# Kernel tuning notes

Measured on AMD Instinct MI355X. Metric: run time of the kernel, lower is better.

## Reference

```python
import jax, jax.numpy as jnp
import numpy as np

B = 16384
N_NODES = 55
N = B * N_NODES
IN_CH = 13
HID = 32
MAX_NBR = 6
N_LAYERS = 5
E = 4 * N


def _sage(x, src, dst, wl, bl, wr, n):
    # PyG SAGEConv: out = lin_l(mean_j x_j) + lin_r(x_i); lin_l has bias, lin_r does not.
    msgs = x[src]                                                   # [E, d]
    agg = jax.ops.segment_sum(msgs, dst, num_segments=n)            # [N, d]
    cnt = jax.ops.segment_sum(jnp.ones((src.shape[0],), x.dtype), dst, num_segments=n)
    agg = agg / jnp.maximum(cnt, 1.0)[:, None]
    return agg @ wl + bl + x @ wr


def setup_inputs() -> dict:
    key = jax.random.key(0)
    ks = jax.random.split(key, 24)
    x = jax.random.normal(ks[0], (N, IN_CH), dtype=jnp.float32)
    # column -3 (index 10) is a binary neighbor mask: exactly MAX_NBR ones per graph
    u = jax.random.uniform(ks[1], (B, N_NODES))
    nbr_idx = jnp.argsort(u, axis=1)[:, :MAX_NBR]
    mask = jnp.zeros((B, N_NODES), jnp.float32).at[jnp.arange(B)[:, None], nbr_idx].set(1.0)
    x = x.at[:, IN_CH - 3].set(mask.reshape(-1))
    edge_index = jax.random.randint(ks[2], (2, E), 0, N, dtype=jnp.int64)
    shuffle_indices = jax.random.randint(ks[3], (B, MAX_NBR), 0, MAX_NBR, dtype=jnp.int64)
    s = 0.1
    wl0 = jax.random.normal(ks[4], (IN_CH, HID)) * s
    bl0 = jnp.zeros((HID,), jnp.float32)
    wr0 = jax.random.normal(ks[5], (IN_CH, HID)) * s
    wl = jax.random.normal(ks[6], (N_LAYERS - 1, HID, HID)) * s
    bl = jnp.zeros((N_LAYERS - 1, HID), jnp.float32)
    wr = jax.random.normal(ks[7], (N_LAYERS - 1, HID, HID)) * s
    wq = jax.random.normal(ks[8], (HID, HID)) * s
    bq = jnp.zeros((HID,), jnp.float32)
    wk = jax.random.normal(ks[9], (HID, HID)) * s
    bk = jnp.zeros((HID,), jnp.float32)
    wv = jax.random.normal(ks[10], (HID, HID)) * s
    bv = jnp.zeros((HID,), jnp.float32)
    wo = jax.random.normal(ks[11], (HID, HID)) * s
    bo = jnp.zeros((HID,), jnp.float32)
    w_fc = jax.random.normal(ks[12], (HID * MAX_NBR, MAX_NBR)) * s
    b_fc = jnp.zeros((MAX_NBR,), jnp.float32)
    return {"x": x, "edge_index": edge_index, "shuffle_indices": shuffle_indices,
            "wl0": wl0, "bl0": bl0, "wr0": wr0, "wl": wl, "bl": bl, "wr": wr,
            "wq": wq, "bq": bq, "wk": wk, "bk": bk, "wv": wv, "bv": bv,
            "wo": wo, "bo": bo, "w_fc": w_fc, "b_fc": b_fc}


def reference(x, edge_index, shuffle_indices, wl0, bl0, wr0, wl, bl, wr,
              wq, bq, wk, bk, wv, bv, wo, bo, w_fc, b_fc):
    n = x.shape[0]
    b = n // N_NODES
    src, dst = edge_index[0], edge_index[1]
    nbr_mask = x[:, IN_CH - 3].reshape(b, N_NODES)                  # [B, 55]

    h = jax.nn.selu(_sage(x, src, dst, wl0, bl0, wr0, n))
    jk = h
    for i in range(N_LAYERS - 1):
        h = jax.nn.selu(_sage(h, src, dst, wl[i], bl[i], wr[i], n))
        jk = jnp.maximum(jk, h)                                     # JumpingKnowledge('max')

    h = jax.nn.selu(jk)                                             # [N, HID]
    keys = h.reshape(b, N_NODES, HID)
    values = keys

    # dynamic neighbor gather: indices of mask==1 in ascending order, zero-padded to MAX_NBR
    order = jnp.argsort(-nbr_mask, axis=1, stable=True)[:, :MAX_NBR]  # [B, 6]
    barange = jnp.arange(b)[:, None]
    query = keys[barange, order]                                    # [B, 6, HID]
    valid = jnp.take_along_axis(nbr_mask, order, axis=1) > 0.5      # [B, 6] bool
    query = jnp.where(valid[..., None], query, 0.0)
    query = query[barange, shuffle_indices]                         # shuffled gather

    # single-head cross attention (head_dim = HID)
    Q = query @ wq + bq
    K = keys @ wk + bk
    V = values @ wv + bv
    scores = jnp.einsum('bqd,bkd->bqk', Q, K) / jnp.sqrt(jnp.float32(HID))
    attn = jax.nn.softmax(scores, axis=-1)
    out = jnp.einsum('bqk,bkd->bqd', attn, V) @ wo + bo             # [B, 6, HID]

    out = jax.nn.selu(out.reshape(b, HID * MAX_NBR))
    return out @ w_fc + b_fc                                        # [B, 6]
```

## Files before the change

kernel.cpp:

```cpp
#include <hip/hip_runtime.h>
#include <cstdint>
#include <cstddef>

#define NODES   55
#define BGRAPH  16384
#define NTOT    (BGRAPH*NODES)
#define INCH    13
#define HID     32
#define ETOT    (4*NTOT)
#define NPB     128
#define ECAP    768
#define ZN      NTOT

#define NBUCK   220
#define BSH     12
#define BMSK    4095
#define NBLK    2048
#define BCAP2   32
#define BINTH   256
#define BINGRP  (ETOT/4/NBLK)
#define OVFCAP  8192

#define ASTR    72
#define BSTR    72
#define ASTR0   40
#define WKV_OFF 9216

#define MODE_A  0
#define MODE_D  2
#define MODE_B  3
#define MODE_C  4

typedef _Float16 f16;
typedef _Float16 f16x4 __attribute__((ext_vector_type(4)));
typedef _Float16 f16x8 __attribute__((ext_vector_type(8)));
typedef float    f32x4 __attribute__((ext_vector_type(4)));
typedef uint32_t u32x4 __attribute__((ext_vector_type(4)));

__device__ __forceinline__ float selu_f(float v){
  const float s  = 1.0507009873554805f;
  const float sa = 1.7580993408473766f;
  return v > 0.f ? s*v : sa*(__expf(v)-1.f);
}

__global__ __launch_bounds__(256) void k_pad(const float* __restrict__ x,
                                             f16* __restrict__ xh,
                                             f16* __restrict__ ha,
                                             f16* __restrict__ hb,
                                             int* __restrict__ ocnt){
  if (blockIdx.x == 0){
    int t = threadIdx.x;
    if (t == 0) *ocnt = 0;
    if (t < 16)                  xh[(size_t)ZN*16 + t]      = (f16)0.f;
    else if (t >= 16 && t < 48)  ha[(size_t)ZN*32 + (t-16)] = (f16)0.f;
    else if (t >= 48 && t < 80)  hb[(size_t)ZN*32 + (t-48)] = (f16)0.f;
  }
  int i = blockIdx.x*256 + threadIdx.x;
  int node = i>>2, q = i&3;
  const float* r = x + (size_t)node*INCH + q*4;
  f16x4 v;
  v[0] = (f16)r[0];
  v[1] = (q<3) ? (f16)r[1] : (f16)0.f;
  v[2] = (q<3) ? (f16)r[2] : (f16)0.f;
  v[3] = (q<3) ? (f16)r[3] : (f16)0.f;
  *(f16x4*)(xh + (size_t)node*16 + q*4) = v;
}

__global__ __launch_bounds__(256) void k_wprep(
    const float* __restrict__ wl0, const float* __restrict__ wr0,
    const float* __restrict__ wl,  const float* __restrict__ wr,
    const float* __restrict__ wk,  const float* __restrict__ wv,
    f16* __restrict__ wcp)
{
  int t = threadIdx.x;
  for (int i=t; i<1024; i+=256){
    int oc = i>>5, k = i&31;
    float v = 0.f;
    if (k < 13)                 v = wl0[k*HID + oc];
    else if (k >= 16 && k < 29) v = wr0[(k-16)*HID + oc];
    wcp[oc*32 + k] = (f16)v;
  }
  for (int i=t; i<4*2048; i+=256){
    int l = i>>11, r = i&2047, oc = r>>6, k = r&63;
    float v = (k<32) ? wl[l*1024 + k*HID + oc] : wr[l*1024 + (k-32)*HID + oc];
    wcp[1024 + l*2048 + oc*64 + k] = (f16)v;
  }
  for (int i=t; i<2048; i+=256){
    int oc = i>>5, k = i&31;
    float v = (oc < 32) ? wk[k*HID + oc] : wv[k*HID + (oc-32)];
    wcp[WKV_OFF + oc*32 + k] = (f16)v;
  }
}

__global__ __launch_bounds__(BINTH) void k_bin(
    const int* __restrict__ src, const int* __restrict__ dst,
    uint32_t* __restrict__ binned, int* __restrict__ gcnt,
    uint2* __restrict__ ovf, int* __restrict__ ocnt)
{
  __shared__ int lcnt[NBUCK];
  int t = threadIdx.x, bid = blockIdx.x;
  for (int i=t;i<NBUCK;i+=BINTH) lcnt[i]=0;
  __syncthreads();
  const int4* s4 = (const int4*)src;
  const int4* d4 = (const int4*)dst;
  int g0 = bid*BINGRP;
  for (int i=t; i<BINGRP; i+=BINTH){
    int4 s = s4[g0+i];
    int4 d = d4[g0+i];
    #pragma unroll
    for (int j=0;j<4;j++){
      int dd = (&d.x)[j];
      int ss = (&s.x)[j];
      int b  = dd >> BSH;
      uint32_t entry = (uint32_t)ss | ((uint32_t)(dd & BMSK) << 20);
      int pos = atomicAdd(&lcnt[b], 1);
      if (pos < BCAP2) binned[((size_t)b*NBLK + bid)*BCAP2 + pos] = entry;
      else {
        int gp = atomicAdd(ocnt, 1);
        if (gp < OVFCAP) ovf[gp] = make_uint2(entry, (uint32_t)b);
      }
    }
  }
  __syncthreads();
  for (int i=t;i<NBUCK;i+=BINTH){
    int c = lcnt[i]; if (c > BCAP2) c = BCAP2;
    gcnt[bid*NBUCK + i] = c;
  }
}

__global__ __launch_bounds__(256) void k_btot(const int* __restrict__ gcnt,
                                              const uint2* __restrict__ ovf,
                                              const int* __restrict__ ocnt,
                                              int* __restrict__ btot){
  __shared__ int sd[256];
  int b = blockIdx.x, t = threadIdx.x;
  int s = 0;
  for (int i=t;i<NBLK;i+=256) s += gcnt[i*NBUCK + b];
  int oc = *ocnt; if (oc > OVFCAP) oc = OVFCAP;
  for (int j=t;j<oc;j+=256) if (ovf[j].y == (uint32_t)b) s++;
  sd[t]=s; __syncthreads();
  for (int o=128;o>0;o>>=1){ if (t<o) sd[t]+=sd[t+o]; __syncthreads(); }
  if (t==0) btot[b]=sd[0];
}

__global__ __launch_bounds__(256) void k_bscan(const int* __restrict__ btot,
                                               int* __restrict__ bbase){
  __shared__ int sd[256];
  int t = threadIdx.x;
  int v = (t<NBUCK) ? btot[t] : 0;
  sd[t] = v; __syncthreads();
  for (int o=1;o<256;o<<=1){
    int u = (t>=o) ? sd[t-o] : 0;
    __syncthreads();
    sd[t] += u;
    __syncthreads();
  }
  if (t<NBUCK) bbase[t] = sd[t] - v;
}

__global__ __launch_bounds__(1024) void k_bucket(
    const uint32_t* __restrict__ binned, const int* __restrict__ gcnt,
    const int* __restrict__ bbase,
    const uint2* __restrict__ ovf, const int* __restrict__ ocnt,
    int* __restrict__ off, uint32_t* __restrict__ csrp)
{
  __shared__ int hist[4096];
  __shared__ int cnts[NBLK];
  __shared__ int ws[1024];
  int b = blockIdx.x, t = threadIdx.x;
  int base = bbase[b];
  for (int i=t;i<NBLK;i+=1024) cnts[i] = gcnt[i*NBUCK + b];
  #pragma unroll
  for (int i=0;i<4;i++) hist[t+1024*i] = 0;
  int oc = *ocnt; if (oc > OVFCAP) oc = OVFCAP;
  __syncthreads();

  const uint4* bb4 = (const uint4*)(binned + (size_t)b*(NBLK*BCAP2));
  for (int i=t; i<NBLK*BCAP2/4; i+=1024){
    uint4 e = bb4[i];
    int c = cnts[i>>3];
    int s0 = (i&7)*4;
    if (s0   < c) atomicAdd(&hist[(e.x>>20)&BMSK],1);
    if (s0+1 < c) atomicAdd(&hist[(e.y>>20)&BMSK],1);
    if (s0+2 < c) atomicAdd(&hist[(e.z>>20)&BMSK],1);
    if (s0+3 < c) atomicAdd(&hist[(e.w>>20)&BMSK],1);
  }
  for (int j=t;j<oc;j+=1024){
    uint2 pr = ovf[j];
    if (pr.y == (uint32_t)b) atomicAdd(&hist[(pr.x>>20)&BMSK],1);
  }
  __syncthreads();
  int t4 = t*4;
  int s0=hist[t4], s1=hist[t4+1], s2=hist[t4+2], s3=hist[t4+3];
  int sum = s0+s1+s2+s3;
  ws[t] = sum; __syncthreads();
  for (int o=1;o<1024;o<<=1){
    int u = (t>=o) ? ws[t-o] : 0;
    __syncthreads();
    ws[t] += u;
    __syncthreads();
  }
  int ex = ws[t] - sum;
  int p0 = ex, p1 = ex+s0, p2 = ex+s0+s1, p3 = ex+s0+s1+s2;
  hist[t4]=p0; hist[t4+1]=p1; hist[t4+2]=p2; hist[t4+3]=p3;
  int4 ov; ov.x = base+p0; ov.y = base+p1; ov.z = base+p2; ov.w = base+p3;
  ((int4*)(off + (b<<BSH)))[t] = ov;
  if (b == NBUCK-1 && t == 1023) off[NTOT] = ETOT;
  __syncthreads();
  for (int i=t; i<NBLK*BCAP2/4; i+=1024){
    uint4 e = bb4[i];
    int c = cnts[i>>3];
    int s0b = (i&7)*4;
    int p;
    if (s0b   < c){ p = atomicAdd(&hist[(e.x>>20)&BMSK],1); csrp[base+p] = e.x & 0xFFFFFu; }
    if (s0b+1 < c){ p = atomicAdd(&hist[(e.y>>20)&BMSK],1); csrp[base+p] = e.y & 0xFFFFFu; }
    if (s0b+2 < c){ p = atomicAdd(&hist[(e.z>>20)&BMSK],1); csrp[base+p] = e.z & 0xFFFFFu; }
    if (s0b+3 < c){ p = atomicAdd(&hist[(e.w>>20)&BMSK],1); csrp[base+p] = e.w & 0xFFFFFu; }
  }
  for (int j=t;j<oc;j+=1024){
    uint2 pr = ovf[j];
    if (pr.y == (uint32_t)b){
      int p = atomicAdd(&hist[(pr.x>>20)&BMSK],1);
      csrp[base+p] = pr.x & 0xFFFFFu;
    }
  }
}

__global__ __launch_bounds__(256,8) void k_layer0(
    const f16* __restrict__ xh,
    const int* __restrict__ off, const uint32_t* __restrict__ csrp,
    const f16* __restrict__ wcat0, const float* __restrict__ bl0,
    f16* __restrict__ hout)
{
  __shared__ uint32_t ALDS[NPB*(ASTR0/2)];
  __shared__ uint32_t BLDS[32*(ASTR0/2)];
  __shared__ uint32_t EL[ECAP];
  __shared__ int      sOFF[NPB+2];
  __shared__ float    biasL[32];
  int t = threadIdx.x;
  int base = blockIdx.x*NPB;
  int e0 = off[base];
  int e1 = off[base+NPB];
  for (int i=t; i<NPB+1; i+=256) sOFF[i] = off[base+i];
  {
    int lim = (e1-e0) < ECAP ? (e1-e0) : ECAP;
    for (int i=t; i<lim; i+=256) EL[i] = csrp[e0+i];
  }
  if (t < 128){
    int oc = t>>2, kq = (t&3)*8;
    f16x8 wv = *(const f16x8*)(wcat0 + oc*32 + kq);
    *(f16x8*)((f16*)BLDS + oc*ASTR0 + kq) = wv;
  }
  if (t < 32) biasL[t] = bl0[t];
  __syncthreads();

  int c4 = t & 3;
  #pragma unroll
  for (int p=0;p<2;p++){
    int nl = p*64 + (t>>2);
    int node = base + nl;
    f16x4 xown = *(const f16x4*)(xh + (size_t)node*16 + 4u*c4);
    int s = sOFF[nl] - e0;
    int d = sOFF[nl+1] - sOFF[nl];
    float a0=0.f,a1=0.f,a2=0.f,a3=0.f;
    for (int i=0;i<d;i+=4){
      int j0 = s+i;
      uint32_t k0,k1,k2,k3;
      if (j0+3 < ECAP){ k0=EL[j0]; k1=EL[j0+1]; k2=EL[j0+2]; k3=EL[j0+3]; }
      else            { k0=csrp[e0+j0]; k1=csrp[e0+j0+1]; k2=csrp[e0+j0+2]; k3=csrp[e0+j0+3]; }
      k1 = (i+1<d)?k1:(uint32_t)ZN;
      k2 = (i+2<d)?k2:(uint32_t)ZN;
      k3 = (i+3<d)?k3:(uint32_t)ZN;
      f16x4 g0 = *(const f16x4*)(xh + (size_t)k0*16u + 4u*c4);
      f16x4 g1 = *(const f16x4*)(xh + (size_t)k1*16u + 4u*c4);
      f16x4 g2 = *(const f16x4*)(xh + (size_t)k2*16u + 4u*c4);
      f16x4 g3 = *(const f16x4*)(xh + (size_t)k3*16u + 4u*c4);
      a0 += ((float)g0[0]+(float)g1[0]) + ((float)g2[0]+(float)g3[0]);
      a1 += ((float)g0[1]+(float)g1[1]) + ((float)g2[1]+(float)g3[1]);
      a2 += ((float)g0[2]+(float)g1[2]) + ((float)g2[2]+(float)g3[2]);
      a3 += ((float)g0[3]+(float)g1[3]) + ((float)g2[3]+(float)g3[3]);
    }
    float inv = 1.f/(float)(d<1?1:d);
    union { f16 h[4]; uint32_t u[2]; } mp, xp;
    mp.h[0]=(f16)(a0*inv); mp.h[1]=(f16)(a1*inv); mp.h[2]=(f16)(a2*inv); mp.h[3]=(f16)(a3*inv);
    xp.h[0]=xown[0]; xp.h[1]=xown[1]; xp.h[2]=xown[2]; xp.h[3]=xown[3];
    uint32_t* arow = &ALDS[nl*(ASTR0/2)];
    *((uint2*)&arow[2*c4])     = make_uint2(mp.u[0], mp.u[1]);
    *((uint2*)&arow[8 + 2*c4]) = make_uint2(xp.u[0], xp.u[1]);
  }
  __syncthreads();

  int w = t>>6, l = t&63;
  int lrow = l&15, lg = l>>4;
  const f16* Af = (const f16*)ALDS;
  const f16* Bf = (const f16*)BLDS;
  f32x4 D00={0.f,0.f,0.f,0.f}, D01=D00, D10=D00, D11=D00;
  {
    f16x8 af0 = *(const f16x8*)(Af + (32*w+lrow)*ASTR0    + 8*lg);
    f16x8 af1 = *(const f16x8*)(Af + (32*w+16+lrow)*ASTR0 + 8*lg);
    f16x8 bf0 = *(const f16x8*)(Bf + lrow*ASTR0           + 8*lg);
    f16x8 bf1 = *(const f16x8*)(Bf + (16+lrow)*ASTR0      + 8*lg);
    D00 = __builtin_amdgcn_mfma_f32_16x16x32_f16(af0, bf0, D00, 0,0,0);
    D01 = __builtin_amdgcn_mfma_f32_16x16x32_f16(af0, bf1, D01, 0,0,0);
    D10 = __builtin_amdgcn_mfma_f32_16x16x32_f16(af1, bf0, D10, 0,0,0);
    D11 = __builtin_amdgcn_mfma_f32_16x16x32_f16(af1, bf1, D11, 0,0,0);
  }
  __syncthreads();

  f16* ST = (f16*)ALDS;
  #pragma unroll
  for (int j=0;j<4;j++){
    int r0 = 32*w + 4*lg + j, r1 = r0 + 16;
    ST[r0*34 + lrow]      = (f16)selu_f(D00[j] + biasL[lrow]);
    ST[r0*34 + 16 + lrow] = (f16)selu_f(D01[j] + biasL[16+lrow]);
    ST[r1*34 + lrow]      = (f16)selu_f(D10[j] + biasL[lrow]);
    ST[r1*34 + 16 + lrow] = (f16)selu_f(D11[j] + biasL[16+lrow]);
  }
  __syncthreads();

  const uint32_t* STd = (const uint32_t*)ALDS;
  uint4* ho4 = (uint4*)hout;
  int gbase = blockIdx.x*(NPB*HID/8);
  #pragma unroll
  for (int k=0;k<2;k++){
    int cch = t + 256*k;
    int n = cch>>2, m = cch&3;
    int dd = n*17 + m*4;
    uint4 u;
    u.x=STd[dd]; u.y=STd[dd+1]; u.z=STd[dd+2]; u.w=STd[dd+3];
    ho4[gbase+cch] = u;
  }
}

__global__ __launch_bounds__(256,6) void k_layer(
    const f16* __restrict__ hin,
    const int* __restrict__ off, const uint32_t* __restrict__ csrp,
    const f16* __restrict__ wcat, const float* __restrict__ bl,
    f16* __restrict__ hout, f16* __restrict__ jkio, int mode)
{
  __shared__ uint32_t ALDS[NPB*(ASTR/2)];
  __shared__ uint32_t BLDS[32*(BSTR/2)];
  __shared__ uint32_t EL[ECAP];
  __shared__ int      sOFF[NPB+2];
  __shared__ float    biasL[32];
  int t = threadIdx.x;
  int base = blockIdx.x*NPB;
  int e0 = off[base];
  int e1 = off[base+NPB];
  for (int i=t; i<NPB+1; i+=256) sOFF[i] = off[base+i];
  {
    int lim = (e1-e0) < ECAP ? (e1-e0) : ECAP;
    for (int i=t; i<lim; i+=256) EL[i] = csrp[e0+i];
  }
  if (t < 128){
    int oc = t>>2, kq = (t&3)*8;
    f16x8 wv0 = *(const f16x8*)(wcat + oc*64 + kq);
    f16x8 wv1 = *(const f16x8*)(wcat + oc*64 + 32 + kq);
    *(f16x8*)((f16*)BLDS + oc*BSTR + kq)      = wv0;
    *(f16x8*)((f16*)BLDS + oc*BSTR + 32 + kq) = wv1;
  }
  if (t < 32) biasL[t] = bl[t];
  __syncthreads();

  int c4 = t & 3;
  #pragma unroll
  for (int p=0;p<2;p++){
    int nl = p*64 + (t>>2);
    int node = base + nl;
    f16x8 hown = *(const f16x8*)(hin + (size_t)node*HID + 8u*c4);
    int s = sOFF[nl] - e0;
    int d = sOFF[nl+1] - sOFF[nl];
    float a[8];
    #pragma unroll
    for (int r=0;r<8;r++) a[r]=0.f;
    for (int i=0;i<d;i+=4){
      int j0 = s+i;
      uint32_t k0,k1,k2,k3;
      if (j0+3 < ECAP){ k0=EL[j0]; k1=EL[j0+1]; k2=EL[j0+2]; k3=EL[j0+3]; }
      else            { k0=csrp[e0+j0]; k1=csrp[e0+j0+1]; k2=csrp[e0+j0+2]; k3=csrp[e0+j0+3]; }
      k1 = (i+1<d)?k1:(uint32_t)ZN;
      k2 = (i+2<d)?k2:(uint32_t)ZN;
      k3 = (i+3<d)?k3:(uint32_t)ZN;
      f16x8 g0 = *((const f16x8*)(hin + (size_t)k0*32u) + c4);
      f16x8 g1 = *((const f16x8*)(hin + (size_t)k1*32u) + c4);
      f16x8 g2 = *((const f16x8*)(hin + (size_t)k2*32u) + c4);
      f16x8 g3 = *((const f16x8*)(hin + (size_t)k3*32u) + c4);
      #pragma unroll
      for (int r=0;r<8;r++)
        a[r] += ((float)g0[r]+(float)g1[r]) + ((float)g2[r]+(float)g3[r]);
    }
    float inv = 1.f/(float)(d<1?1:d);
    union { f16 h[8]; uint4 v; } mp;
    #pragma unroll
    for (int r=0;r<8;r++) mp.h[r] = (f16)(a[r]*inv);
    uint32_t* arow = &ALDS[nl*(ASTR/2)];
    *((uint4*)&arow[4*c4]) = mp.v;
    *((f16x8*)((f16*)arow + 32 + 8*c4)) = hown;
  }
  __syncthreads();

  int w = t>>6, l = t&63;
  int lrow = l&15, lg = l>>4;
  const f16* Af = (const f16*)ALDS;
  const f16* Bf = (const f16*)BLDS;
  f32x4 D00={0.f,0.f,0.f,0.f}, D01=D00, D10=D00, D11=D00;
  #pragma unroll
  for (int s2=0;s2<2;s2++){
    f16x8 af0 = *(const f16x8*)(Af + (32*w+lrow)*ASTR    + 32*s2 + 8*lg);
    f16x8 af1 = *(const f16x8*)(Af + (32*w+16+lrow)*ASTR + 32*s2 + 8*lg);
    f16x8 bf0 = *(const f16x8*)(Bf + lrow*BSTR           + 32*s2 + 8*lg);
    f16x8 bf1 = *(const f16x8*)(Bf + (16+lrow)*BSTR      + 32*s2 + 8*lg);
    D00 = __builtin_amdgcn_mfma_f32_16x16x32_f16(af0, bf0, D00, 0,0,0);
    D01 = __builtin_amdgcn_mfma_f32_16x16x32_f16(af0, bf1, D01, 0,0,0);
    D10 = __builtin_amdgcn_mfma_f32_16x16x32_f16(af1, bf0, D10, 0,0,0);
    D11 = __builtin_amdgcn_mfma_f32_16x16x32_f16(af1, bf1, D11, 0,0,0);
  }
  __syncthreads();

  f16* ST = (f16*)ALDS;
  #pragma unroll
  for (int j=0;j<4;j++){
    int r0 = 32*w + 4*lg + j, r1 = r0 + 16;
    ST[r0*34 + lrow]      = (f16)selu_f(D00[j] + biasL[lrow]);
    ST[r0*34 + 16 + lrow] = (f16)selu_f(D01[j] + biasL[16+lrow]);
    ST[r1*34 + lrow]      = (f16)selu_f(D10[j] + biasL[lrow]);
    ST[r1*34 + 16 + lrow] = (f16)selu_f(D11[j] + biasL[16+lrow]);
  }
  __syncthreads();

  const uint32_t* STd = (const uint32_t*)ALDS;
  u32x4* ho4 = (u32x4*)hout;
  u32x4* jo4 = (u32x4*)jkio;
  const u32x4* hi4 = (const u32x4*)hin;
  int gbase = blockIdx.x*(NPB*HID/8);
  #pragma unroll
  for (int k=0;k<2;k++){
    int cch = t + 256*k;
    int n = cch>>2, m = cch&3;
    int dd = n*17 + m*4;
    union UU { u32x4 u; f16 hh[8]; };
    UU hv, jv, j2;
    hv.u = (u32x4){STd[dd], STd[dd+1], STd[dd+2], STd[dd+3]};
    if (mode != MODE_B){
      if (mode == MODE_A) jv.u = hi4[gbase+cch];
      else                jv.u = __builtin_nontemporal_load(jo4 + gbase + cch);
      if (mode == MODE_C){
        j2.u = hi4[gbase+cch];
        #pragma unroll
        for (int r=0;r<8;r++) jv.hh[r] = (j2.hh[r] > jv.hh[r]) ? j2.hh[r] : jv.hh[r];
      }
      #pragma unroll
      for (int r=0;r<8;r++) jv.hh[r] = (hv.hh[r] > jv.hh[r]) ? hv.hh[r] : jv.hh[r];
      __builtin_nontemporal_store(jv.u, jo4 + gbase + cch);
    }
    if (mode != MODE_D) ho4[gbase+cch] = hv.u;
  }
}

__global__ __launch_bounds__(256) void k_attn(
    const f16* __restrict__ jk, const float* __restrict__ x,
    const int* __restrict__ shuf, const f16* __restrict__ wkvT,
    const float* __restrict__ wq, const float* __restrict__ bq,
    const float* __restrict__ bk, const float* __restrict__ bv,
    const float* __restrict__ wo, const float* __restrict__ bo,
    const float* __restrict__ wfc, const float* __restrict__ bfc,
    float* __restrict__ out)
{
  __shared__ alignas(16) f16 Ah[64*40];
  __shared__ float K[NODES*33];
  __shared__ float V[NODES*33];
  __shared__ float Qs[6*33];
  __shared__ float S[6*56];
  __shared__ float O[6*33];
  __shared__ float SO[192];
  __shared__ float part[96];
  __shared__ int   sel[8];

  int g = blockIdx.x, t = threadIdx.x;

  {
    const f16x8* j8 = (const f16x8*)(jk + (size_t)g*NODES*HID);
    for (int i=t; i<NODES*HID/8; i+=256){
      f16x8 v = __builtin_nontemporal_load(j8 + i);
      int node = i >> 2, c0 = (i & 3)*8;
      f16x8 hv;
      #pragma unroll
      for (int r=0;r<8;r++) hv[r] = (f16)selu_f((float)v[r]);
      *(f16x8*)(Ah + node*40 + c0) = hv;
    }
  }
  if (t < 64){
    float mv = (t < NODES) ? x[(size_t)(g*NODES+t)*INCH + (INCH-3)] : 0.f;
    unsigned long long mb = __ballot(mv > 0.5f);
    if (t < 6){
      int kk = shuf[g*6 + t];
      for (int i2=0;i2<kk;i2++) mb &= (mb - 1ull);
      sel[t] = (int)__builtin_ctzll(mb);
    }
  }
  __syncthreads();

  {
    int w = t>>6, l = t&63;
    int lrow = l&15, lg = l>>4;
    f16x8 af = *(const f16x8*)(Ah + (16*w + lrow)*40 + 8*lg);
    #pragma unroll
    for (int ct=0; ct<4; ct++){
      f16x8 bf = *(const f16x8*)(wkvT + (16*ct + lrow)*32 + 8*lg);
      f32x4 D = {0.f,0.f,0.f,0.f};
      D = __builtin_amdgcn_mfma_f32_16x16x32_f16(af, bf, D, 0,0,0);
      int ocl = 16*(ct&1) + lrow;
      float bias = (ct < 2) ? bk[ocl] : bv[ocl];
      float* dst = (ct < 2) ? K : V;
      #pragma unroll
      for (int j=0;j<4;j++){
        int node = 16*w + 4*lg + j;
        if (node < NODES) dst[node*33 + ocl] = D[j] + bias;
      }
    }
  }
  if (t < 192){
    int q = t>>5, oc = t&31;
    int node = sel[q];
    const f16x8* hr8 = (const f16x8*)(Ah + node*40);
    float a = bq[oc];
    #pragma unroll
    for (int cc=0;cc<4;cc++){
      f16x8 hv = hr8[cc];
      #pragma unroll
      for (int r=0;r<8;r++) a = fmaf((float)hv[r], wq[(8*cc+r)*HID + oc], a);
    }
    Qs[q*33+oc] = a;
  }
  __syncthreads();

  for (int idx=t; idx<6*NODES; idx+=256){
    int q = idx % 6, k = idx / 6;
    float a = 0.f;
    #pragma unroll
    for (int c=0;c<HID;c++) a = fmaf(Qs[q*33+c], K[k*33+c], a);
    S[q*56+k] = a * 0.17677669529663687f;
  }
  __syncthreads();

  if (t < 192){
    int q = t>>5, l = t&31;
    float v0 = (l      < NODES) ? S[q*56+l]    : -1e30f;
    float v1 = (l+32   < NODES) ? S[q*56+l+32] : -1e30f;
    float mx = fmaxf(v0, v1);
    #pragma unroll
    for (int o=16;o>0;o>>=1) mx = fmaxf(mx, __shfl_xor(mx, o, 32));
    float p0 = (l    < NODES) ? __expf(v0-mx) : 0.f;
    float p1 = (l+32 < NODES) ? __expf(v1-mx) : 0.f;
    float sm = p0 + p1;
    #pragma unroll
    for (int o=16;o>0;o>>=1) sm += __shfl_xor(sm, o, 32);
    float inv = 1.f/sm;
    if (l    < NODES) S[q*56+l]    = p0*inv;
    if (l+32 < NODES) S[q*56+l+32] = p1*inv;
  }
  __syncthreads();

  if (t < 192){
    int q = t>>5, oc = t&31;
    float a = 0.f;
    for (int k=0;k<NODES;k++) a = fmaf(S[q*56+k], V[k*33+oc], a);
    O[q*33+oc] = a;
  }
  __syncthreads();

  if (t < 192){
    int q = t>>5, oc = t&31;
    float a = bo[oc];
    #pragma unroll
    for (int c=0;c<HID;c++) a = fmaf(O[q*33+c], wo[c*HID+oc], a);
    SO[t] = selu_f(a);
  }
  __syncthreads();

  if (t < 96){
    int j = t % 6, pp = t / 6;
    float a = 0.f;
    #pragma unroll
    for (int r=0;r<12;r++) a = fmaf(SO[pp*12+r], wfc[(pp*12+r)*6+j], a);
    part[pp*6+j] = a;
  }
  __syncthreads();
  if (t < 6){
    float a = bfc[t];
    #pragma unroll
    for (int pp=0;pp<16;pp++) a += part[pp*6+t];
    out[g*6+t] = a;
  }
}

extern "C" void kernel_launch(void* const* d_in, const int* in_sizes, int n_in,
                              void* d_out, int out_size, void* d_ws, size_t ws_size,
                              hipStream_t stream)
{
  const float* x   = (const float*)d_in[0];
  const int*   eix = (const int*)d_in[1];
  const int*   shf = (const int*)d_in[2];
  const float* wl0 = (const float*)d_in[3];
  const float* bl0 = (const float*)d_in[4];
  const float* wr0 = (const float*)d_in[5];
  const float* wl  = (const float*)d_in[6];
  const float* bl  = (const float*)d_in[7];
  const float* wr  = (const float*)d_in[8];
  const float* wq  = (const float*)d_in[9];
  const float* bq  = (const float*)d_in[10];
  const float* wk  = (const float*)d_in[11];
  const float* bk  = (const float*)d_in[12];
  const float* wv  = (const float*)d_in[13];
  const float* bv  = (const float*)d_in[14];
  const float* wo  = (const float*)d_in[15];
  const float* bo  = (const float*)d_in[16];
  const float* wfc = (const float*)d_in[17];
  const float* bfc = (const float*)d_in[18];
  float* out = (float*)d_out;

  const int* esrc = eix;
  const int* edst = eix + ETOT;

  char* p = (char*)d_ws;
  auto carve = [&](size_t bytes){ void* r = (void*)p; p += (bytes + 255) & ~(size_t)255; return r; };
  int*      off   = (int*)carve(sizeof(int)*(NTOT+1));
  int*      gcnt  = (int*)carve(sizeof(int)*(size_t)NBLK*NBUCK);
  int*      btot  = (int*)carve(sizeof(int)*256);
  int*      bbase = (int*)carve(sizeof(int)*256);
  uint2*    ovf   = (uint2*)carve(sizeof(uint2)*OVFCAP);
  int*      ocnt  = (int*)carve(sizeof(int)*64);
  f16*      wcp   = (f16*)carve(sizeof(f16)*(WKV_OFF + 2048));
  uint32_t* csrp  = (uint32_t*)carve(sizeof(uint32_t)*((size_t)ETOT + 64));
  f16*      h_a   = (f16*)carve(2*((size_t)NTOT+1)*HID);
  f16*      h_b   = (f16*)carve(2*((size_t)NTOT+1)*HID);
  f16*      jk16  = (f16*)carve(2*(size_t)NTOT*HID);

  f16*      xh     = (f16*)h_b;
  uint32_t* binned = (uint32_t*)h_a;

  k_pad   <<<ETOT/256,  256, 0, stream>>>(x, xh, h_a, h_b, ocnt);
  k_wprep <<<1,         256, 0, stream>>>(wl0, wr0, wl, wr, wk, wv, wcp);
  k_bin   <<<NBLK,    BINTH, 0, stream>>>(esrc, edst, binned, gcnt, ovf, ocnt);
  k_btot  <<<NBUCK,     256, 0, stream>>>(gcnt, ovf, ocnt, btot);
  k_bscan <<<1,         256, 0, stream>>>(btot, bbase);
  k_bucket<<<NBUCK,    1024, 0, stream>>>(binned, gcnt, bbase, ovf, ocnt, off, csrp);

  k_layer0<<<NTOT/NPB, 256, 0, stream>>>(xh, off, csrp, wcp, bl0, h_a);
  f16* hc = h_a; f16* hn = h_b;
  static const int modes[4] = {MODE_A, MODE_B, MODE_C, MODE_D};
  for (int l=0; l<4; l++){
    k_layer<<<NTOT/NPB, 256, 0, stream>>>(hc, off, csrp,
                                          wcp + 1024 + l*2048, bl + l*HID,
                                          hn, jk16, modes[l]);
    f16* tmp = hc; hc = hn; hn = tmp;
  }
  k_attn<<<BGRAPH, 256, 0, stream>>>(jk16, x, shf, wcp + WKV_OFF,
                                     wq, bq, bk, bv, wo, bo, wfc, bfc, out);
}
```

Baseline: 811.3 us.

## Shrink layer kernel LDS, read weights from global, raise occupancy

The SAGE layer kernel drops the separate LDS copy of the weight matrix and loads MFMA B-fragments straight from global memory. It also removes the row padding on the A tile and shrinks the edge-list cache from 768 to 640 entries, which cuts LDS per block so the launch bound can go from 6 to 8 blocks per CU. Separately, the JK and attention loads and stores switch from nontemporal builtins back to ordinary accesses. The unpadded 64-element A rows may cause LDS bank conflicts. More edges per block may now spill to the slower global fallback path, and weight loads become per-wave global reads.

```diff
diff --git a/kernel.cpp b/kernel.cpp
--- a/kernel.cpp
+++ b/kernel.cpp
@@ -10,6 +10,7 @@
 #define ETOT    (4*NTOT)
 #define NPB     128
 #define ECAP    768
+#define ECAP2   640
 #define ZN      NTOT
 
 #define NBUCK   220
@@ -21,8 +22,6 @@
 #define BINGRP  (ETOT/4/NBLK)
 #define OVFCAP  8192
 
-#define ASTR    72
-#define BSTR    72
 #define ASTR0   40
 #define WKV_OFF 9216
 
@@ -35,7 +34,6 @@
 typedef _Float16 f16x4 __attribute__((ext_vector_type(4)));
 typedef _Float16 f16x8 __attribute__((ext_vector_type(8)));
 typedef float    f32x4 __attribute__((ext_vector_type(4)));
-typedef uint32_t u32x4 __attribute__((ext_vector_type(4)));
 
 __device__ __forceinline__ float selu_f(float v){
   const float s  = 1.0507009873554805f;
@@ -332,15 +330,14 @@
   }
 }
 
-__global__ __launch_bounds__(256,6) void k_layer(
+__global__ __launch_bounds__(256,8) void k_layer(
     const f16* __restrict__ hin,
     const int* __restrict__ off, const uint32_t* __restrict__ csrp,
     const f16* __restrict__ wcat, const float* __restrict__ bl,
     f16* __restrict__ hout, f16* __restrict__ jkio, int mode)
 {
-  __shared__ uint32_t ALDS[NPB*(ASTR/2)];
-  __shared__ uint32_t BLDS[32*(BSTR/2)];
-  __shared__ uint32_t EL[ECAP];
+  __shared__ uint32_t ALDS[NPB*32];
+  __shared__ uint32_t EL[ECAP2];
   __shared__ int      sOFF[NPB+2];
   __shared__ float    biasL[32];
   int t = threadIdx.x;
@@ -349,15 +346,8 @@
   int e1 = off[base+NPB];
   for (int i=t; i<NPB+1; i+=256) sOFF[i] = off[base+i];
   {
-    int lim = (e1-e0) < ECAP ? (e1-e0) : ECAP;
+    int lim = (e1-e0) < ECAP2 ? (e1-e0) : ECAP2;
     for (int i=t; i<lim; i+=256) EL[i] = csrp[e0+i];
-  }
-  if (t < 128){
-    int oc = t>>2, kq = (t&3)*8;
-    f16x8 wv0 = *(const f16x8*)(wcat + oc*64 + kq);
-    f16x8 wv1 = *(const f16x8*)(wcat + oc*64 + 32 + kq);
-    *(f16x8*)((f16*)BLDS + oc*BSTR + kq)      = wv0;
-    *(f16x8*)((f16*)BLDS + oc*BSTR + 32 + kq) = wv1;
   }
   if (t < 32) biasL[t] = bl[t];
   __syncthreads();
@@ -376,8 +366,8 @@
     for (int i=0;i<d;i+=4){
       int j0 = s+i;
       uint32_t k0,k1,k2,k3;
-      if (j0+3 < ECAP){ k0=EL[j0]; k1=EL[j0+1]; k2=EL[j0+2]; k3=EL[j0+3]; }
-      else            { k0=csrp[e0+j0]; k1=csrp[e0+j0+1]; k2=csrp[e0+j0+2]; k3=csrp[e0+j0+3]; }
+      if (j0+3 < ECAP2){ k0=EL[j0]; k1=EL[j0+1]; k2=EL[j0+2]; k3=EL[j0+3]; }
+      else             { k0=csrp[e0+j0]; k1=csrp[e0+j0+1]; k2=csrp[e0+j0+2]; k3=csrp[e0+j0+3]; }
       k1 = (i+1<d)?k1:(uint32_t)ZN;
       k2 = (i+2<d)?k2:(uint32_t)ZN;
       k3 = (i+3<d)?k3:(uint32_t)ZN;
@@ -393,7 +383,7 @@
     union { f16 h[8]; uint4 v; } mp;
     #pragma unroll
     for (int r=0;r<8;r++) mp.h[r] = (f16)(a[r]*inv);
-    uint32_t* arow = &ALDS[nl*(ASTR/2)];
+    uint32_t* arow = &ALDS[nl*32];
     *((uint4*)&arow[4*c4]) = mp.v;
     *((f16x8*)((f16*)arow + 32 + 8*c4)) = hown;
   }
@@ -402,14 +392,13 @@
   int w = t>>6, l = t&63;
   int lrow = l&15, lg = l>>4;
   const f16* Af = (const f16*)ALDS;
-  const f16* Bf = (const f16*)BLDS;
   f32x4 D00={0.f,0.f,0.f,0.f}, D01=D00, D10=D00, D11=D00;
   #pragma unroll
   for (int s2=0;s2<2;s2++){
-    f16x8 af0 = *(const f16x8*)(Af + (32*w+lrow)*ASTR    + 32*s2 + 8*lg);
-    f16x8 af1 = *(const f16x8*)(Af + (32*w+16+lrow)*ASTR + 32*s2 + 8*lg);
-    f16x8 bf0 = *(const f16x8*)(Bf + lrow*BSTR           + 32*s2 + 8*lg);
-    f16x8 bf1 = *(const f16x8*)(Bf + (16+lrow)*BSTR      + 32*s2 + 8*lg);
+    f16x8 af0 = *(const f16x8*)(Af + (32*w+lrow)*64    + 32*s2 + 8*lg);
+    f16x8 af1 = *(const f16x8*)(Af + (32*w+16+lrow)*64 + 32*s2 + 8*lg);
+    f16x8 bf0 = *(const f16x8*)(wcat + lrow*64         + 32*s2 + 8*lg);
+    f16x8 bf1 = *(const f16x8*)(wcat + (16+lrow)*64    + 32*s2 + 8*lg);
     D00 = __builtin_amdgcn_mfma_f32_16x16x32_f16(af0, bf0, D00, 0,0,0);
     D01 = __builtin_amdgcn_mfma_f32_16x16x32_f16(af0, bf1, D01, 0,0,0);
     D10 = __builtin_amdgcn_mfma_f32_16x16x32_f16(af1, bf0, D10, 0,0,0);
@@ -429,21 +418,21 @@
   __syncthreads();
 
   const uint32_t* STd = (const uint32_t*)ALDS;
-  u32x4* ho4 = (u32x4*)hout;
-  u32x4* jo4 = (u32x4*)jkio;
-  const u32x4* hi4 = (const u32x4*)hin;
+  uint4* ho4 = (uint4*)hout;
+  uint4* jo4 = (uint4*)jkio;
+  const uint4* hi4 = (const uint4*)hin;
   int gbase = blockIdx.x*(NPB*HID/8);
   #pragma unroll
   for (int k=0;k<2;k++){
     int cch = t + 256*k;
     int n = cch>>2, m = cch&3;
     int dd = n*17 + m*4;
-    union UU { u32x4 u; f16 hh[8]; };
+    union UU { uint4 u; f16 hh[8]; };
     UU hv, jv, j2;
-    hv.u = (u32x4){STd[dd], STd[dd+1], STd[dd+2], STd[dd+3]};
+    hv.u.x=STd[dd]; hv.u.y=STd[dd+1]; hv.u.z=STd[dd+2]; hv.u.w=STd[dd+3];
     if (mode != MODE_B){
       if (mode == MODE_A) jv.u = hi4[gbase+cch];
-      else                jv.u = __builtin_nontemporal_load(jo4 + gbase + cch);
+      else                jv.u = jo4[gbase+cch];
       if (mode == MODE_C){
         j2.u = hi4[gbase+cch];
         #pragma unroll
@@ -451,7 +440,7 @@
       }
       #pragma unroll
       for (int r=0;r<8;r++) jv.hh[r] = (hv.hh[r] > jv.hh[r]) ? hv.hh[r] : jv.hh[r];
-      __builtin_nontemporal_store(jv.u, jo4 + gbase + cch);
+      jo4[gbase+cch] = jv.u;
     }
     if (mode != MODE_D) ho4[gbase+cch] = hv.u;
   }
@@ -481,7 +470,7 @@
   {
     const f16x8* j8 = (const f16x8*)(jk + (size_t)g*NODES*HID);
     for (int i=t; i<NODES*HID/8; i+=256){
-      f16x8 v = __builtin_nontemporal_load(j8 + i);
+      f16x8 v = j8[i];
       int node = i >> 2, c0 = (i & 3)*8;
       f16x8 hv;
       #pragma unroll
```

After: 810.7 us. Within noise of the previous version (-0.1%).
